# Kernel tuning notes

Measured on AMD Instinct MI355X. Metric: run time of the kernel, lower is better.

## Reference

```python
import jax, jax.numpy as jnp
import numpy as np

STEPS_PER_PIECE = 4  # fixed-step RK4 substeps per spline piece (stands in for the adaptive solver)


def setup_inputs() -> dict:
    key = jax.random.key(0)
    ks = jax.random.split(key, 10)
    B, P, C, H, O = 4096, 64, 128, 128, 10  # batch, spline pieces, channels(=latent), hidden, output
    rn = lambda k, sh: jax.random.normal(k, sh, dtype=jnp.float32)
    return {
        "z0": rn(ks[0], (B, C)),
        # Hermite-cubic spline coefficients per piece: X(s) = a + b s + c s^2 + d s^3
        "coeffs": rn(ks[1], (B, P, C, 4)) * 0.05,
        "W1": rn(ks[2], (C, H)) / np.sqrt(C).astype(np.float32),
        "b1": jnp.zeros((H,), jnp.float32),
        "W2": rn(ks[3], (H, H)) / np.sqrt(H).astype(np.float32),
        "b2": jnp.zeros((H,), jnp.float32),
        "W3": rn(ks[4], (H, C)) / np.sqrt(H).astype(np.float32),
        "b3": jnp.zeros((C,), jnp.float32),
        "Wr": rn(ks[5], (H, O)) / np.sqrt(H).astype(np.float32),
        "br": jnp.zeros((O,), jnp.float32),
    }


def reference(z0, coeffs, W1, b1, W2, b2, W3, b3, Wr, br):
    P = coeffs.shape[1]
    n_steps = P * STEPS_PER_PIECE
    dt = jnp.float32(1.0 / STEPS_PER_PIECE)  # spline piece i covers t in [i, i+1]

    def dXdt(t):
        # derivative of the cubic spline at scalar time t -> [B, C]
        idx = jnp.clip(jnp.floor(t).astype(jnp.int32), 0, P - 1)
        s = t - idx.astype(t.dtype)
        c = jax.lax.dynamic_index_in_dim(coeffs, idx, axis=1, keepdims=False)  # [B, C, 4]
        return c[..., 1] + (2.0 * c[..., 2] + 3.0 * c[..., 3] * s) * s

    def f(z):
        # CDEFunc: Linear -> ELU -> Linear -> ReLU -> Linear
        h = jax.nn.elu(z @ W1 + b1)
        h = jax.nn.relu(h @ W2 + b2)
        return h @ W3 + b3

    def rk4_step(z, t):
        k1 = f(z) * dXdt(t)
        k2 = f(z + 0.5 * dt * k1) * dXdt(t + 0.5 * dt)
        k3 = f(z + 0.5 * dt * k2) * dXdt(t + 0.5 * dt)
        k4 = f(z + dt * k3) * dXdt(t + dt)
        z = z + (dt / 6.0) * (k1 + 2.0 * k2 + 2.0 * k3 + k4)
        return z, None

    ts = jnp.arange(n_steps, dtype=jnp.float32) * dt
    zT, _ = jax.lax.scan(rk4_step, z0, ts)  # terminal latent state = zt[:, 1]
    return zT @ Wr + br
```

## Files before the change

kernel.cpp:

```cpp
#include <hip/hip_runtime.h>
#include <hip/hip_bf16.h>
#include <math.h>


typedef short bf16x8 __attribute__((ext_vector_type(8)));
typedef float f32x4  __attribute__((ext_vector_type(4)));
typedef unsigned int u32x2 __attribute__((ext_vector_type(2)));

#define MFMA16(a, b, c) __builtin_amdgcn_mfma_f32_16x16x32_bf16((a), (b), (c), 0, 0, 0)

__device__ __forceinline__ unsigned short f2bf(float x) {
  unsigned int u = __float_as_uint(x);
  u += 0x7FFFu + ((u >> 16) & 1u);
  return (unsigned short)(u >> 16);
}

__device__ __forceinline__ unsigned int cvt_pk(float lo, float hi) {
  unsigned int r;
  asm("v_cvt_pk_bf16_f32 %0, %1, %2" : "=v"(r) : "v"(lo), "v"(hi));
  return r;
}

__device__ __forceinline__ void barrier_lgkm() {
  asm volatile("s_waitcnt lgkmcnt(0)" ::: "memory");
  __builtin_amdgcn_s_barrier();
  asm volatile("" ::: "memory");
}

__global__ __launch_bounds__(256, 1) void cde_fused(
    const float* __restrict__ z0, const float* __restrict__ coeffs,
    const float* __restrict__ W1, const float* __restrict__ b1,
    const float* __restrict__ W2, const float* __restrict__ b2,
    const float* __restrict__ W3, const float* __restrict__ b3,
    const float* __restrict__ Wr, const float* __restrict__ br,
    float* __restrict__ out) {
  __shared__ __align__(16) unsigned short zbuf[2][16][136];
  char* const lds = (char*)&zbuf[0][0][0];

  const int tid  = (int)threadIdx.x;
  const int lane = tid & 63;
  const int wv   = tid >> 6;
  const int l15  = lane & 15;
  const int q    = lane >> 4;
  const int cb0  = wv * 32;
  const int row0 = (int)blockIdx.x * 16;

  const int rdbyte = l15 * 272 + q * 16;
  const int wrbyte0 = l15 * 272 + (cb0 + 4 * q) * 2;
  const int wrbyte1 = wrbyte0 + 32;

  bf16x8 wf1[2][4], wf2[2][4], wf3[2][4];
#pragma unroll
  for (int mt = 0; mt < 2; ++mt) {
    const int col = cb0 + 16 * mt + l15;
#pragma unroll
    for (int ks = 0; ks < 4; ++ks) {
      bf16x8 fa, fb, fc;
#pragma unroll
      for (int i = 0; i < 8; ++i) {
        const int k = ks * 32 + q * 8 + i;
        fa[i] = (short)f2bf(W1[k * 128 + col]);
        fb[i] = (short)f2bf(W2[k * 128 + col]);
        fc[i] = (short)f2bf(W3[k * 128 + col]);
      }
      wf1[mt][ks] = fa; wf2[mt][ks] = fb; wf3[mt][ks] = fc;
    }
  }
  f32x4 bv1[2], bv2[2], bv3[2];
#pragma unroll
  for (int mt = 0; mt < 2; ++mt) {
    bv1[mt] = *(const f32x4*)(b1 + cb0 + 16 * mt + 4 * q);
    bv2[mt] = *(const f32x4*)(b2 + cb0 + 16 * mt + 4 * q);
    bv3[mt] = *(const f32x4*)(b3 + cb0 + 16 * mt + 4 * q);
  }

  f32x4 cf[8];
  auto coeff_load = [&](int p) {
    const float* cb = coeffs + ((size_t)(row0 + l15) * 64 + p) * 512;
#pragma unroll
    for (int mt = 0; mt < 2; ++mt)
#pragma unroll
      for (int r = 0; r < 4; ++r)
        cf[mt * 4 + r] = *(const f32x4*)(cb + (cb0 + 16 * mt + 4 * q + r) * 4);
  };
  float c1v[8], c2b[8], c3b[8];
  auto coeff_adopt = [&]() {
#pragma unroll
    for (int e = 0; e < 8; ++e) {
      c1v[e] = cf[e][1]; c2b[e] = 2.f * cf[e][2]; c3b[e] = 3.f * cf[e][3];
    }
  };

  auto stv = [&](int wb, const float (&h)[8]) {
    u32x2 w0, w1;
    w0[0] = cvt_pk(h[0], h[1]); w0[1] = cvt_pk(h[2], h[3]);
    w1[0] = cvt_pk(h[4], h[5]); w1[1] = cvt_pk(h[6], h[7]);
    *(u32x2*)(lds + (wb * 4352 + wrbyte0)) = w0;
    *(u32x2*)(lds + (wb * 4352 + wrbyte1)) = w1;
  };

  float zr[8];
  {
    const float* zp = z0 + (size_t)(row0 + l15) * 128;
    const f32x4 za = *(const f32x4*)(zp + cb0 + 4 * q);
    const f32x4 zb = *(const f32x4*)(zp + cb0 + 16 + 4 * q);
#pragma unroll
    for (int r = 0; r < 4; ++r) { zr[r] = za[r]; zr[4 + r] = zb[r]; }
  }
  coeff_load(0);
  coeff_adopt();
  {
    float h[8];
#pragma unroll
    for (int e = 0; e < 8; ++e) h[e] = zr[e];
    stv(0, h);
  }
  barrier_lgkm();

  float kx[8], sacc[8], dxb[8];

  auto layer = [&](const bf16x8(&wf)[2][4], const f32x4(&bias)[2], int rb,
                   f32x4& A0, f32x4& A1) {
    const char* base = lds + rb * 4352 + rdbyte;
    bf16x8 x0 = *(const bf16x8*)(base);
    bf16x8 x1 = *(const bf16x8*)(base + 64);
    bf16x8 x2 = *(const bf16x8*)(base + 128);
    bf16x8 x3 = *(const bf16x8*)(base + 192);
    A0 = bias[0]; A1 = bias[1];
    A0 = MFMA16(wf[0][0], x0, A0); A1 = MFMA16(wf[1][0], x0, A1);
    A0 = MFMA16(wf[0][1], x1, A0); A1 = MFMA16(wf[1][1], x1, A1);
    A0 = MFMA16(wf[0][2], x2, A0); A1 = MFMA16(wf[1][2], x2, A1);
    A0 = MFMA16(wf[0][3], x3, A0); A1 = MFMA16(wf[1][3], x3, A1);
  };

  auto run_f = [&](int sp) {
    f32x4 A0, A1;
    float h[8];
    layer(wf1, bv1, sp, A0, A1);
#pragma unroll
    for (int r = 0; r < 4; ++r) {
      h[r]     = fmaxf(A0[r], __expf(fminf(A0[r], 0.f)) - 1.f);
      h[4 + r] = fmaxf(A1[r], __expf(fminf(A1[r], 0.f)) - 1.f);
    }
    stv(sp ^ 1, h);
    barrier_lgkm();
    layer(wf2, bv2, sp ^ 1, A0, A1);
#pragma unroll
    for (int r = 0; r < 4; ++r) {
      h[r] = fmaxf(A0[r], 0.f); h[4 + r] = fmaxf(A1[r], 0.f);
    }
    stv(sp, h);
    barrier_lgkm();
    layer(wf3, bv3, sp, A0, A1);
#pragma unroll
    for (int r = 0; r < 4; ++r) { kx[r] = A0[r]; kx[4 + r] = A1[r]; }
  };

#pragma unroll 1
  for (int p = 0; p < 64; ++p) {
    const bool pre = p < 63;
    if (pre) coeff_load(p + 1);

#pragma unroll
    for (int sub = 0; sub < 4; ++sub) {
      const float s0 = 0.25f * (float)sub;

      run_f(0);
      {
        float h[8];
#pragma unroll
        for (int e = 0; e < 8; ++e) {
          const float dx = c1v[e] + (c2b[e] + c3b[e] * s0) * s0;
          kx[e] *= dx; sacc[e] = kx[e];
          h[e] = zr[e] + 0.125f * kx[e];
        }
        stv(1, h);
      }
      barrier_lgkm();

      run_f(1);
      {
        const float sb = s0 + 0.125f;
        float h[8];
#pragma unroll
        for (int e = 0; e < 8; ++e) {
          dxb[e] = c1v[e] + (c2b[e] + c3b[e] * sb) * sb;
          kx[e] *= dxb[e]; sacc[e] += 2.f * kx[e];
          h[e] = zr[e] + 0.125f * kx[e];
        }
        stv(0, h);
      }
      barrier_lgkm();

      run_f(0);
      {
        float h[8];
#pragma unroll
        for (int e = 0; e < 8; ++e) {
          kx[e] *= dxb[e]; sacc[e] += 2.f * kx[e];
          h[e] = zr[e] + 0.25f * kx[e];
        }
        stv(1, h);
      }
      barrier_lgkm();

      run_f(1);
      if (sub == 3) {
        if (pre) {
#pragma unroll
          for (int e = 0; e < 8; ++e) kx[e] *= cf[e][1];
        } else {
#pragma unroll
          for (int e = 0; e < 8; ++e) kx[e] *= (c1v[e] + c2b[e] + c3b[e]);
        }
      } else {
        const float sc = s0 + 0.25f;
#pragma unroll
        for (int e = 0; e < 8; ++e)
          kx[e] *= c1v[e] + (c2b[e] + c3b[e] * sc) * sc;
      }
      {
        float h[8];
#pragma unroll
        for (int e = 0; e < 8; ++e) {
          sacc[e] += kx[e];
          zr[e] += (0.25f / 6.f) * sacc[e];
          h[e] = zr[e];
        }
        stv(0, h);
      }
      barrier_lgkm();
    }
    if (pre) coeff_adopt();
  }

  {
    float* zf = (float*)lds;
    *(f32x4*)(zf + l15 * 132 + cb0 + 4 * q)      = f32x4{zr[0], zr[1], zr[2], zr[3]};
    *(f32x4*)(zf + l15 * 132 + cb0 + 16 + 4 * q) = f32x4{zr[4], zr[5], zr[6], zr[7]};
  }
  barrier_lgkm();
  if (tid < 160) {
    const int row = tid / 10, o = tid - row * 10;
    const float* zf = (const float*)lds;
    float acc = br[o];
#pragma unroll 4
    for (int ch = 0; ch < 128; ++ch)
      acc = fmaf(zf[row * 132 + ch], Wr[ch * 10 + o], acc);
    out[(size_t)(row0 + row) * 10 + o] = acc;
  }
}

extern "C" void kernel_launch(void* const* d_in, const int* in_sizes, int n_in,
                              void* d_out, int out_size, void* d_ws, size_t ws_size,
                              hipStream_t stream) {
  const float* z0     = (const float*)d_in[0];
  const float* coeffs = (const float*)d_in[1];
  const float* W1 = (const float*)d_in[2]; const float* b1 = (const float*)d_in[3];
  const float* W2 = (const float*)d_in[4]; const float* b2 = (const float*)d_in[5];
  const float* W3 = (const float*)d_in[6]; const float* b3 = (const float*)d_in[7];
  const float* Wr = (const float*)d_in[8]; const float* br = (const float*)d_in[9];
  hipLaunchKernelGGL(cde_fused, dim3(256), dim3(256), 0, stream,
                     z0, coeffs, W1, b1, W2, b2, W3, b3, Wr, br, (float*)d_out);
}
```

Baseline: 804.8 us.

## Give each wave its own rows and full weights to remove block barriers

Each wave now handles 4 batch rows across all 128 channels, keeping all three weight matrices as bf16 MFMA fragments in registers. Layer activations are re-packed in registers as the next layer's MFMA operands, so block-wide barriers and shared-memory round trips between layers disappear. Only a small per-wave shared-memory exchange remains, for the k-vector and the state. The cost is four times the MFMA work per wave, since 12 of the 16 MFMA columns are padding. Register pressure also rises sharply and may cause spilling.

```diff
diff --git a/kernel.cpp b/kernel.cpp
--- a/kernel.cpp
+++ b/kernel.cpp
@@ -5,7 +5,9 @@
 
 typedef short bf16x8 __attribute__((ext_vector_type(8)));
 typedef float f32x4  __attribute__((ext_vector_type(4)));
+typedef float f32x2  __attribute__((ext_vector_type(2)));
 typedef unsigned int u32x2 __attribute__((ext_vector_type(2)));
+typedef unsigned int u32x4 __attribute__((ext_vector_type(4)));
 
 #define MFMA16(a, b, c) __builtin_amdgcn_mfma_f32_16x16x32_bf16((a), (b), (c), 0, 0, 0)
 
@@ -21,10 +23,9 @@
   return r;
 }
 
-__device__ __forceinline__ void barrier_lgkm() {
+__device__ __forceinline__ void lgkm0_fence() {
   asm volatile("s_waitcnt lgkmcnt(0)" ::: "memory");
-  __builtin_amdgcn_s_barrier();
-  asm volatile("" ::: "memory");
+  __builtin_amdgcn_sched_barrier(0);
 }
 
 __global__ __launch_bounds__(256, 1) void cde_fused(
@@ -34,215 +35,235 @@
     const float* __restrict__ W3, const float* __restrict__ b3,
     const float* __restrict__ Wr, const float* __restrict__ br,
     float* __restrict__ out) {
-  __shared__ __align__(16) unsigned short zbuf[2][16][136];
-  char* const lds = (char*)&zbuf[0][0][0];
+  __shared__ __align__(16) char lds_all[4 * 4224 + 1536];
 
   const int tid  = (int)threadIdx.x;
   const int lane = tid & 63;
   const int wv   = tid >> 6;
   const int l15  = lane & 15;
   const int q    = lane >> 4;
-  const int cb0  = wv * 32;
+  const int rl   = lane & 3;
+  const int oct  = lane >> 2;
   const int row0 = (int)blockIdx.x * 16;
-
-  const int rdbyte = l15 * 272 + q * 16;
-  const int wrbyte0 = l15 * 272 + (cb0 + 4 * q) * 2;
-  const int wrbyte1 = wrbyte0 + 32;
-
-  bf16x8 wf1[2][4], wf2[2][4], wf3[2][4];
-#pragma unroll
-  for (int mt = 0; mt < 2; ++mt) {
-    const int col = cb0 + 16 * mt + l15;
+  const int grow = row0 + wv * 4 + rl;
+
+  char* const wb = lds_all + wv * 4224;
+  char* const kx = wb + 1088;
+  float* const biasD = (float*)(lds_all + 4 * 4224);
+
+  const int zrd  = (l15 & 3) * 272 + 8 * q;
+  const int zwr  = rl * 272 + oct * 16;
+  const int kxo  = 16 * q + 16 * (q >> 1);
+  const int kwrb = l15 * 784;
+  const int krd  = rl * 784 + oct * 48;
+
+  if (wv == 0) {
+    for (int j = lane; j < 384; j += 64) {
+      const float* bs = (j < 128) ? b1 : (j < 256 ? b2 : b3);
+      biasD[j] = bs[j & 127];
+    }
+  }
+
+  bf16x8 wfA[8][4], wfB[8][4], wfC[8][4];
+  {
+    auto build = [&](const float* Wsrc, bf16x8(&dst)[8][4]) {
+#pragma unroll
+      for (int mt = 0; mt < 8; ++mt)
+#pragma unroll
+        for (int ks = 0; ks < 4; ++ks) {
+          bf16x8 f;
+#pragma unroll
+          for (int i = 0; i < 8; ++i) {
+            const int j = 4 * ks + (i >> 1);
+            const int h = 16 * (j >> 1) + 4 * q + 2 * (j & 1) + (i & 1);
+            f[i] = (short)f2bf(Wsrc[h * 128 + 16 * mt + l15]);
+          }
+          dst[mt][ks] = f;
+        }
+    };
+    build(W1, wfA);
+    build(W2, wfB);
+    build(W3, wfC);
+  }
+
+  float z[8];
+  {
+    const float* zp = z0 + (size_t)grow * 128 + oct * 8;
+    const f32x4 a = *(const f32x4*)zp;
+    const f32x4 b = *(const f32x4*)(zp + 4);
+#pragma unroll
+    for (int e = 0; e < 4; ++e) { z[e] = a[e]; z[4 + e] = b[e]; }
+  }
+  float c1v[8], c2b[8], c3b[8];
+  {
+    const float* cb = coeffs + (size_t)grow * 64 * 512 + oct * 32;
+#pragma unroll
+    for (int jc = 0; jc < 8; ++jc) {
+      const f32x2 c23 = *(const f32x2*)(cb + jc * 4 + 2);
+      c1v[jc] = cb[jc * 4 + 1];
+      c2b[jc] = 2.f * c23[0];
+      c3b[jc] = 3.f * c23[1];
+    }
+  }
+  {
+    u32x4 t;
+#pragma unroll
+    for (int k2 = 0; k2 < 4; ++k2) t[k2] = cvt_pk(z[2 * k2], z[2 * k2 + 1]);
+    *(u32x4*)(wb + zwr) = t;
+  }
+  __syncthreads();
+
+  auto Lmm = [&](const bf16x8(&wf)[8][4], int bo, const bf16x8(&xk)[4],
+                 f32x4(&acc)[8]) {
+#pragma unroll
+    for (int mt = 0; mt < 8; ++mt)
+      acc[mt] = *(const f32x4*)(biasD + bo + 16 * mt + 4 * q);
+#pragma unroll
+    for (int ks = 0; ks < 4; ++ks)
+#pragma unroll
+      for (int mt = 0; mt < 8; ++mt)
+        acc[mt] = MFMA16(wf[mt][ks], xk[ks], acc[mt]);
+  };
+
+  auto run3 = [&](f32x4(&acc)[8]) {
+    bf16x8 xk[4];
 #pragma unroll
     for (int ks = 0; ks < 4; ++ks) {
-      bf16x8 fa, fb, fc;
-#pragma unroll
-      for (int i = 0; i < 8; ++i) {
-        const int k = ks * 32 + q * 8 + i;
-        fa[i] = (short)f2bf(W1[k * 128 + col]);
-        fb[i] = (short)f2bf(W2[k * 128 + col]);
-        fc[i] = (short)f2bf(W3[k * 128 + col]);
-      }
-      wf1[mt][ks] = fa; wf2[mt][ks] = fb; wf3[mt][ks] = fc;
-    }
-  }
-  f32x4 bv1[2], bv2[2], bv3[2];
-#pragma unroll
-  for (int mt = 0; mt < 2; ++mt) {
-    bv1[mt] = *(const f32x4*)(b1 + cb0 + 16 * mt + 4 * q);
-    bv2[mt] = *(const f32x4*)(b2 + cb0 + 16 * mt + 4 * q);
-    bv3[mt] = *(const f32x4*)(b3 + cb0 + 16 * mt + 4 * q);
-  }
-
-  f32x4 cf[8];
-  auto coeff_load = [&](int p) {
-    const float* cb = coeffs + ((size_t)(row0 + l15) * 64 + p) * 512;
-#pragma unroll
-    for (int mt = 0; mt < 2; ++mt)
-#pragma unroll
-      for (int r = 0; r < 4; ++r)
-        cf[mt * 4 + r] = *(const f32x4*)(cb + (cb0 + 16 * mt + 4 * q + r) * 4);
-  };
-  float c1v[8], c2b[8], c3b[8];
-  auto coeff_adopt = [&]() {
-#pragma unroll
-    for (int e = 0; e < 8; ++e) {
-      c1v[e] = cf[e][1]; c2b[e] = 2.f * cf[e][2]; c3b[e] = 3.f * cf[e][3];
-    }
-  };
-
-  auto stv = [&](int wb, const float (&h)[8]) {
-    u32x2 w0, w1;
-    w0[0] = cvt_pk(h[0], h[1]); w0[1] = cvt_pk(h[2], h[3]);
-    w1[0] = cvt_pk(h[4], h[5]); w1[1] = cvt_pk(h[6], h[7]);
-    *(u32x2*)(lds + (wb * 4352 + wrbyte0)) = w0;
-    *(u32x2*)(lds + (wb * 4352 + wrbyte1)) = w1;
-  };
-
-  float zr[8];
-  {
-    const float* zp = z0 + (size_t)(row0 + l15) * 128;
-    const f32x4 za = *(const f32x4*)(zp + cb0 + 4 * q);
-    const f32x4 zb = *(const f32x4*)(zp + cb0 + 16 + 4 * q);
-#pragma unroll
-    for (int r = 0; r < 4; ++r) { zr[r] = za[r]; zr[4 + r] = zb[r]; }
-  }
-  coeff_load(0);
-  coeff_adopt();
-  {
-    float h[8];
-#pragma unroll
-    for (int e = 0; e < 8; ++e) h[e] = zr[e];
-    stv(0, h);
-  }
-  barrier_lgkm();
-
-  float kx[8], sacc[8], dxb[8];
-
-  auto layer = [&](const bf16x8(&wf)[2][4], const f32x4(&bias)[2], int rb,
-                   f32x4& A0, f32x4& A1) {
-    const char* base = lds + rb * 4352 + rdbyte;
-    bf16x8 x0 = *(const bf16x8*)(base);
-    bf16x8 x1 = *(const bf16x8*)(base + 64);
-    bf16x8 x2 = *(const bf16x8*)(base + 128);
-    bf16x8 x3 = *(const bf16x8*)(base + 192);
-    A0 = bias[0]; A1 = bias[1];
-    A0 = MFMA16(wf[0][0], x0, A0); A1 = MFMA16(wf[1][0], x0, A1);
-    A0 = MFMA16(wf[0][1], x1, A0); A1 = MFMA16(wf[1][1], x1, A1);
-    A0 = MFMA16(wf[0][2], x2, A0); A1 = MFMA16(wf[1][2], x2, A1);
-    A0 = MFMA16(wf[0][3], x3, A0); A1 = MFMA16(wf[1][3], x3, A1);
-  };
-
-  auto run_f = [&](int sp) {
-    f32x4 A0, A1;
-    float h[8];
-    layer(wf1, bv1, sp, A0, A1);
-#pragma unroll
-    for (int r = 0; r < 4; ++r) {
-      h[r]     = fmaxf(A0[r], __expf(fminf(A0[r], 0.f)) - 1.f);
-      h[4 + r] = fmaxf(A1[r], __expf(fminf(A1[r], 0.f)) - 1.f);
-    }
-    stv(sp ^ 1, h);
-    barrier_lgkm();
-    layer(wf2, bv2, sp ^ 1, A0, A1);
-#pragma unroll
-    for (int r = 0; r < 4; ++r) {
-      h[r] = fmaxf(A0[r], 0.f); h[4 + r] = fmaxf(A1[r], 0.f);
-    }
-    stv(sp, h);
-    barrier_lgkm();
-    layer(wf3, bv3, sp, A0, A1);
-#pragma unroll
-    for (int r = 0; r < 4; ++r) { kx[r] = A0[r]; kx[4 + r] = A1[r]; }
-  };
-
+      const u32x2 lo = *(const u32x2*)(wb + zrd + ks * 64);
+      const u32x2 hi = *(const u32x2*)(wb + zrd + ks * 64 + 32);
+      u32x4 t; t[0] = lo[0]; t[1] = lo[1]; t[2] = hi[0]; t[3] = hi[1];
+      xk[ks] = __builtin_bit_cast(bf16x8, t);
+    }
+    Lmm(wfA, 0, xk, acc);
+    {
+      unsigned int d[16];
+#pragma unroll
+      for (int j = 0; j < 16; ++j) {
+        float a = acc[j >> 1][2 * (j & 1)], b = acc[j >> 1][2 * (j & 1) + 1];
+        a = fmaxf(a, __expf(fminf(a, 0.f)) - 1.f);
+        b = fmaxf(b, __expf(fminf(b, 0.f)) - 1.f);
+        d[j] = cvt_pk(a, b);
+      }
+#pragma unroll
+      for (int ks = 0; ks < 4; ++ks) {
+        u32x4 t; t[0]=d[4*ks]; t[1]=d[4*ks+1]; t[2]=d[4*ks+2]; t[3]=d[4*ks+3];
+        xk[ks] = __builtin_bit_cast(bf16x8, t);
+      }
+    }
+    Lmm(wfB, 128, xk, acc);
+    {
+      unsigned int d[16];
+#pragma unroll
+      for (int j = 0; j < 16; ++j)
+        d[j] = cvt_pk(fmaxf(acc[j >> 1][2 * (j & 1)], 0.f),
+                      fmaxf(acc[j >> 1][2 * (j & 1) + 1], 0.f));
+#pragma unroll
+      for (int ks = 0; ks < 4; ++ks) {
+        u32x4 t; t[0]=d[4*ks]; t[1]=d[4*ks+1]; t[2]=d[4*ks+2]; t[3]=d[4*ks+3];
+        xk[ks] = __builtin_bit_cast(bf16x8, t);
+      }
+    }
+    Lmm(wfC, 256, xk, acc);
+  };
+
+  auto kx_trip = [&](const f32x4(&acc)[8], float(&kd)[8]) {
+    if (l15 < 4) {
+#pragma unroll
+      for (int mt = 0; mt < 8; ++mt)
+        *(f32x4*)(kx + kwrb + 96 * mt + kxo) = acc[mt];
+    }
+    lgkm0_fence();
+    const f32x4 ka = *(const f32x4*)(kx + krd);
+    const f32x4 kb = *(const f32x4*)(kx + krd + 16);
+#pragma unroll
+    for (int e = 0; e < 4; ++e) { kd[e] = ka[e]; kd[4 + e] = kb[e]; }
+  };
+
+  auto zx_write = [&](const float(&v)[8]) {
+    u32x4 t;
+#pragma unroll
+    for (int k2 = 0; k2 < 4; ++k2) t[k2] = cvt_pk(v[2 * k2], v[2 * k2 + 1]);
+    *(u32x4*)(wb + zwr) = t;
+    lgkm0_fence();
+  };
+
+  float zacc[8];
 #pragma unroll 1
   for (int p = 0; p < 64; ++p) {
-    const bool pre = p < 63;
-    if (pre) coeff_load(p + 1);
-
-#pragma unroll
+#pragma unroll 1
     for (int sub = 0; sub < 4; ++sub) {
       const float s0 = 0.25f * (float)sub;
-
-      run_f(0);
+#pragma unroll
+      for (int e = 0; e < 8; ++e) zacc[e] = z[e];
+
+#pragma unroll 1
+      for (int st = 0; st < 3; ++st) {
+        const float s  = s0 + (st ? 0.125f : 0.0f);
+        const float ah = (st == 2) ? 0.25f : 0.125f;
+        const float wz = (st == 0) ? (0.25f / 6.f) : (0.5f / 6.f);
+        f32x4 acc[8];
+        run3(acc);
+        float kd[8];
+        kx_trip(acc, kd);
+        float h[8];
+#pragma unroll
+        for (int e = 0; e < 8; ++e) {
+          const float dx = c1v[e] + (c2b[e] + c3b[e] * s) * s;
+          const float k = kd[e] * dx;
+          zacc[e] += wz * k;
+          h[e] = z[e] + ah * k;
+        }
+        zx_write(h);
+      }
+
       {
-        float h[8];
+        f32x4 acc[8];
+        run3(acc);
+        float kd[8];
+        kx_trip(acc, kd);
+        float dxm[8];
+        if (sub < 3) {
+          const float sc = s0 + 0.25f;
+#pragma unroll
+          for (int e = 0; e < 8; ++e)
+            dxm[e] = c1v[e] + (c2b[e] + c3b[e] * sc) * sc;
+        } else if (p < 63) {
+          const float* cb = coeffs + ((size_t)grow * 64 + (p + 1)) * 512 + oct * 32;
+#pragma unroll
+          for (int jc = 0; jc < 8; ++jc) {
+            const f32x2 c23 = *(const f32x2*)(cb + jc * 4 + 2);
+            const float c1n = cb[jc * 4 + 1];
+            c1v[jc] = c1n;
+            c2b[jc] = 2.f * c23[0];
+            c3b[jc] = 3.f * c23[1];
+            dxm[jc] = c1n;
+          }
+        } else {
+#pragma unroll
+          for (int e = 0; e < 8; ++e) dxm[e] = c1v[e] + c2b[e] + c3b[e];
+        }
+        float zn[8];
 #pragma unroll
         for (int e = 0; e < 8; ++e) {
-          const float dx = c1v[e] + (c2b[e] + c3b[e] * s0) * s0;
-          kx[e] *= dx; sacc[e] = kx[e];
-          h[e] = zr[e] + 0.125f * kx[e];
-        }
-        stv(1, h);
-      }
-      barrier_lgkm();
-
-      run_f(1);
-      {
-        const float sb = s0 + 0.125f;
-        float h[8];
-#pragma unroll
-        for (int e = 0; e < 8; ++e) {
-          dxb[e] = c1v[e] + (c2b[e] + c3b[e] * sb) * sb;
-          kx[e] *= dxb[e]; sacc[e] += 2.f * kx[e];
-          h[e] = zr[e] + 0.125f * kx[e];
-        }
-        stv(0, h);
-      }
-      barrier_lgkm();
-
-      run_f(0);
-      {
-        float h[8];
-#pragma unroll
-        for (int e = 0; e < 8; ++e) {
-          kx[e] *= dxb[e]; sacc[e] += 2.f * kx[e];
-          h[e] = zr[e] + 0.25f * kx[e];
-        }
-        stv(1, h);
-      }
-      barrier_lgkm();
-
-      run_f(1);
-      if (sub == 3) {
-        if (pre) {
-#pragma unroll
-          for (int e = 0; e < 8; ++e) kx[e] *= cf[e][1];
-        } else {
-#pragma unroll
-          for (int e = 0; e < 8; ++e) kx[e] *= (c1v[e] + c2b[e] + c3b[e]);
-        }
-      } else {
-        const float sc = s0 + 0.25f;
-#pragma unroll
-        for (int e = 0; e < 8; ++e)
-          kx[e] *= c1v[e] + (c2b[e] + c3b[e] * sc) * sc;
-      }
-      {
-        float h[8];
-#pragma unroll
-        for (int e = 0; e < 8; ++e) {
-          sacc[e] += kx[e];
-          zr[e] += (0.25f / 6.f) * sacc[e];
-          h[e] = zr[e];
-        }
-        stv(0, h);
-      }
-      barrier_lgkm();
-    }
-    if (pre) coeff_adopt();
-  }
-
-  {
-    float* zf = (float*)lds;
-    *(f32x4*)(zf + l15 * 132 + cb0 + 4 * q)      = f32x4{zr[0], zr[1], zr[2], zr[3]};
-    *(f32x4*)(zf + l15 * 132 + cb0 + 16 + 4 * q) = f32x4{zr[4], zr[5], zr[6], zr[7]};
-  }
-  barrier_lgkm();
+          const float k = kd[e] * dxm[e];
+          z[e] = zacc[e] + (0.25f / 6.f) * k;
+          zn[e] = z[e];
+        }
+        zx_write(zn);
+      }
+    }
+  }
+
+  __syncthreads();
+  {
+    float* zf = (float*)lds_all;
+    *(f32x4*)(zf + (wv * 4 + rl) * 132 + oct * 8)     = f32x4{z[0], z[1], z[2], z[3]};
+    *(f32x4*)(zf + (wv * 4 + rl) * 132 + oct * 8 + 4) = f32x4{z[4], z[5], z[6], z[7]};
+  }
+  __syncthreads();
   if (tid < 160) {
     const int row = tid / 10, o = tid - row * 10;
-    const float* zf = (const float*)lds;
+    const float* zf = (const float*)lds_all;
     float acc = br[o];
 #pragma unroll 4
     for (int ch = 0; ch < 128; ++ch)
```

Measured after the change: 2.533 ms. 215% more time.

## Permute K layout so each wave consumes its own slice before the barrier

Applied to the files above, without the earlier changes.

Remaps the weight K-index permutation so each wave's own output chunk (8 contiguous channels per lane) forms exactly one MFMA K-slice. Each wave issues the MFMAs for its own slice from registers before the barrier, then reads the other three slices from LDS after it. The write becomes a single 16-byte store, and the accumulation is split into two chains to shorten the MFMA dependency chain. The aim is to hide barrier and LDS latency behind useful MFMA work on the serial 3-layer RK4 critical path, at the cost of an extra vector add per layer.

```diff
diff --git a/kernel.cpp b/kernel.cpp
--- a/kernel.cpp
+++ b/kernel.cpp
@@ -5,9 +5,11 @@
 
 typedef short bf16x8 __attribute__((ext_vector_type(8)));
 typedef float f32x4  __attribute__((ext_vector_type(4)));
-typedef unsigned int u32x2 __attribute__((ext_vector_type(2)));
-
-#define MFMA16(a, b, c) __builtin_amdgcn_mfma_f32_16x16x32_bf16((a), (b), (c), 0, 0, 0)
+typedef unsigned int u32x4 __attribute__((ext_vector_type(4)));
+
+__device__ __forceinline__ f32x4 MFMA16(bf16x8 a, bf16x8 b, f32x4 c) {
+  return __builtin_amdgcn_mfma_f32_16x16x32_bf16(a, b, c, 0, 0, 0);
+}
 
 __device__ __forceinline__ unsigned short f2bf(float x) {
   unsigned int u = __float_as_uint(x);
@@ -35,30 +37,32 @@
     const float* __restrict__ Wr, const float* __restrict__ br,
     float* __restrict__ out) {
   __shared__ __align__(16) unsigned short zbuf[2][16][136];
-  char* const lds = (char*)&zbuf[0][0][0];
+  char* const lds = (char*)zbuf;
 
   const int tid  = (int)threadIdx.x;
   const int lane = tid & 63;
   const int wv   = tid >> 6;
   const int l15  = lane & 15;
   const int q    = lane >> 4;
-  const int cb0  = wv * 32;
   const int row0 = (int)blockIdx.x * 16;
 
-  const int rdbyte = l15 * 272 + q * 16;
-  const int wrbyte0 = l15 * 272 + (cb0 + 4 * q) * 2;
-  const int wrbyte1 = wrbyte0 + 32;
+  const f32x4 ZERO4 = {0.f, 0.f, 0.f, 0.f};
+
+  const int exb  = l15 * 272 + 16 * q;
+  const int ownb = exb + 64 * wv;
+  const int ks1 = (wv + 1) & 3, ks2 = (wv + 2) & 3, ks3 = (wv + 3) & 3;
+  const int off1 = exb + 64 * ks1, off2 = exb + 64 * ks2, off3 = exb + 64 * ks3;
 
   bf16x8 wf1[2][4], wf2[2][4], wf3[2][4];
 #pragma unroll
   for (int mt = 0; mt < 2; ++mt) {
-    const int col = cb0 + 16 * mt + l15;
+    const int col = 32 * wv + 16 * mt + l15;
 #pragma unroll
     for (int ks = 0; ks < 4; ++ks) {
       bf16x8 fa, fb, fc;
 #pragma unroll
       for (int i = 0; i < 8; ++i) {
-        const int k = ks * 32 + q * 8 + i;
+        const int k = 32 * ks + 16 * (i >> 2) + 4 * q + (i & 3);
         fa[i] = (short)f2bf(W1[k * 128 + col]);
         fb[i] = (short)f2bf(W2[k * 128 + col]);
         fc[i] = (short)f2bf(W3[k * 128 + col]);
@@ -69,9 +73,9 @@
   f32x4 bv1[2], bv2[2], bv3[2];
 #pragma unroll
   for (int mt = 0; mt < 2; ++mt) {
-    bv1[mt] = *(const f32x4*)(b1 + cb0 + 16 * mt + 4 * q);
-    bv2[mt] = *(const f32x4*)(b2 + cb0 + 16 * mt + 4 * q);
-    bv3[mt] = *(const f32x4*)(b3 + cb0 + 16 * mt + 4 * q);
+    bv1[mt] = *(const f32x4*)(b1 + 32 * wv + 16 * mt + 4 * q);
+    bv2[mt] = *(const f32x4*)(b2 + 32 * wv + 16 * mt + 4 * q);
+    bv3[mt] = *(const f32x4*)(b3 + 32 * wv + 16 * mt + 4 * q);
   }
 
   f32x4 cf[8];
@@ -81,7 +85,7 @@
     for (int mt = 0; mt < 2; ++mt)
 #pragma unroll
       for (int r = 0; r < 4; ++r)
-        cf[mt * 4 + r] = *(const f32x4*)(cb + (cb0 + 16 * mt + 4 * q + r) * 4);
+        cf[mt * 4 + r] = *(const f32x4*)(cb + (32 * wv + 16 * mt + 4 * q + r) * 4);
   };
   float c1v[8], c2b[8], c3b[8];
   auto coeff_adopt = [&]() {
@@ -91,21 +95,22 @@
     }
   };
 
-  auto stv = [&](int wb, const float (&h)[8]) {
-    u32x2 w0, w1;
-    w0[0] = cvt_pk(h[0], h[1]); w0[1] = cvt_pk(h[2], h[3]);
-    w1[0] = cvt_pk(h[4], h[5]); w1[1] = cvt_pk(h[6], h[7]);
-    *(u32x2*)(lds + (wb * 4352 + wrbyte0)) = w0;
-    *(u32x2*)(lds + (wb * 4352 + wrbyte1)) = w1;
+  u32x4 zb;
+  auto emit = [&](const float(&h)[8], int wbuf) {
+    u32x4 t;
+    t[0] = cvt_pk(h[0], h[1]); t[1] = cvt_pk(h[2], h[3]);
+    t[2] = cvt_pk(h[4], h[5]); t[3] = cvt_pk(h[6], h[7]);
+    zb = t;
+    *(u32x4*)(lds + wbuf * 4352 + ownb) = t;
   };
 
   float zr[8];
   {
-    const float* zp = z0 + (size_t)(row0 + l15) * 128;
-    const f32x4 za = *(const f32x4*)(zp + cb0 + 4 * q);
-    const f32x4 zb = *(const f32x4*)(zp + cb0 + 16 + 4 * q);
-#pragma unroll
-    for (int r = 0; r < 4; ++r) { zr[r] = za[r]; zr[4 + r] = zb[r]; }
+    const float* zp = z0 + (size_t)(row0 + l15) * 128 + 32 * wv + 4 * q;
+    const f32x4 za = *(const f32x4*)zp;
+    const f32x4 zc = *(const f32x4*)(zp + 16);
+#pragma unroll
+    for (int r = 0; r < 4; ++r) { zr[r] = za[r]; zr[4 + r] = zc[r]; }
   }
   coeff_load(0);
   coeff_adopt();
@@ -113,24 +118,28 @@
     float h[8];
 #pragma unroll
     for (int e = 0; e < 8; ++e) h[e] = zr[e];
-    stv(0, h);
-  }
-  barrier_lgkm();
+    emit(h, 0);
+  }
 
   float kx[8], sacc[8], dxb[8];
 
-  auto layer = [&](const bf16x8(&wf)[2][4], const f32x4(&bias)[2], int rb,
+  auto layer = [&](const bf16x8(&wf)[2][4], const f32x4(&bv)[2], int rb,
                    f32x4& A0, f32x4& A1) {
-    const char* base = lds + rb * 4352 + rdbyte;
-    bf16x8 x0 = *(const bf16x8*)(base);
-    bf16x8 x1 = *(const bf16x8*)(base + 64);
-    bf16x8 x2 = *(const bf16x8*)(base + 128);
-    bf16x8 x3 = *(const bf16x8*)(base + 192);
-    A0 = bias[0]; A1 = bias[1];
-    A0 = MFMA16(wf[0][0], x0, A0); A1 = MFMA16(wf[1][0], x0, A1);
-    A0 = MFMA16(wf[0][1], x1, A0); A1 = MFMA16(wf[1][1], x1, A1);
-    A0 = MFMA16(wf[0][2], x2, A0); A1 = MFMA16(wf[1][2], x2, A1);
-    A0 = MFMA16(wf[0][3], x3, A0); A1 = MFMA16(wf[1][3], x3, A1);
+    const bf16x8 xo = __builtin_bit_cast(bf16x8, zb);
+    f32x4 P0 = MFMA16(wf[0][wv], xo, bv[0]);
+    f32x4 P1 = MFMA16(wf[1][wv], xo, bv[1]);
+    barrier_lgkm();
+    const char* base = lds + rb * 4352;
+    const bf16x8 x1 = *(const bf16x8*)(base + off1);
+    const bf16x8 x2 = *(const bf16x8*)(base + off2);
+    const bf16x8 x3 = *(const bf16x8*)(base + off3);
+    P0 = MFMA16(wf[0][ks1], x1, P0);
+    P1 = MFMA16(wf[1][ks1], x1, P1);
+    f32x4 Q0 = MFMA16(wf[0][ks2], x2, ZERO4);
+    f32x4 Q1 = MFMA16(wf[1][ks2], x2, ZERO4);
+    Q0 = MFMA16(wf[0][ks3], x3, Q0);
+    Q1 = MFMA16(wf[1][ks3], x3, Q1);
+    A0 = P0 + Q0; A1 = P1 + Q1;
   };
 
   auto run_f = [&](int sp) {
@@ -142,15 +151,13 @@
       h[r]     = fmaxf(A0[r], __expf(fminf(A0[r], 0.f)) - 1.f);
       h[4 + r] = fmaxf(A1[r], __expf(fminf(A1[r], 0.f)) - 1.f);
     }
-    stv(sp ^ 1, h);
-    barrier_lgkm();
+    emit(h, sp ^ 1);
     layer(wf2, bv2, sp ^ 1, A0, A1);
 #pragma unroll
     for (int r = 0; r < 4; ++r) {
       h[r] = fmaxf(A0[r], 0.f); h[4 + r] = fmaxf(A1[r], 0.f);
     }
-    stv(sp, h);
-    barrier_lgkm();
+    emit(h, sp);
     layer(wf3, bv3, sp, A0, A1);
 #pragma unroll
     for (int r = 0; r < 4; ++r) { kx[r] = A0[r]; kx[4 + r] = A1[r]; }
@@ -174,9 +181,8 @@
           kx[e] *= dx; sacc[e] = kx[e];
           h[e] = zr[e] + 0.125f * kx[e];
         }
-        stv(1, h);
-      }
-      barrier_lgkm();
+        emit(h, 1);
+      }
 
       run_f(1);
       {
@@ -188,9 +194,8 @@
           kx[e] *= dxb[e]; sacc[e] += 2.f * kx[e];
           h[e] = zr[e] + 0.125f * kx[e];
         }
-        stv(0, h);
-      }
-      barrier_lgkm();
+        emit(h, 0);
+      }
 
       run_f(0);
       {
@@ -200,9 +205,8 @@
           kx[e] *= dxb[e]; sacc[e] += 2.f * kx[e];
           h[e] = zr[e] + 0.25f * kx[e];
         }
-        stv(1, h);
-      }
-      barrier_lgkm();
+        emit(h, 1);
+      }
 
       run_f(1);
       if (sub == 3) {
@@ -227,19 +231,19 @@
           zr[e] += (0.25f / 6.f) * sacc[e];
           h[e] = zr[e];
         }
-        stv(0, h);
-      }
-      barrier_lgkm();
+        emit(h, 0);
+      }
     }
     if (pre) coeff_adopt();
   }
 
+  __syncthreads();
   {
     float* zf = (float*)lds;
-    *(f32x4*)(zf + l15 * 132 + cb0 + 4 * q)      = f32x4{zr[0], zr[1], zr[2], zr[3]};
-    *(f32x4*)(zf + l15 * 132 + cb0 + 16 + 4 * q) = f32x4{zr[4], zr[5], zr[6], zr[7]};
-  }
-  barrier_lgkm();
+    *(f32x4*)(zf + l15 * 132 + 32 * wv + 4 * q)      = f32x4{zr[0], zr[1], zr[2], zr[3]};
+    *(f32x4*)(zf + l15 * 132 + 32 * wv + 16 + 4 * q) = f32x4{zr[4], zr[5], zr[6], zr[7]};
+  }
+  __syncthreads();
   if (tid < 160) {
     const int row = tid / 10, o = tid - row * 10;
     const float* zf = (const float*)lds;
```

After: 933.8 us. +16.0%, slower.
